# Kernel optimization log

Measured on AMD Instinct MI355X. Metric: run time of the kernel, lower is better.

Reference implementation:

```python
import jax, jax.numpy as jnp
import numpy as np

M = 16       # learned queries
K = 64       # top-k sparse tokens
HEADS = 4    # attention heads
LN_EPS = 1e-5


def _l2norm(x, eps=1e-12):
    n = jnp.linalg.norm(x, axis=-1, keepdims=True)
    return x / jnp.maximum(n, eps)


def _layernorm(x, w, b):
    mu = x.mean(-1, keepdims=True)
    var = x.var(-1, keepdims=True)
    return (x - mu) * jax.lax.rsqrt(var + LN_EPS) * w + b


def setup_inputs() -> dict:
    key = jax.random.key(0)
    ks = jax.random.split(key, 12)
    B, N, C, T, TD, D = 4, 16384, 1024, 20, 512, 64
    s = lambda k, sh: jax.random.normal(k, sh, jnp.float32) * 0.02
    return {
        "image_features": jax.random.normal(ks[0], (B, N, C), jnp.float32),
        "text_features": jax.random.normal(ks[1], (B, T, TD), jnp.float32),
        "Wd": s(ks[2], (C, D)), "bd": jnp.zeros((D,), jnp.float32),
        "Wu": s(ks[3], (D, C)), "bu": jnp.zeros((C,), jnp.float32),
        "m_queries": jax.random.normal(ks[4], (1, M, D), jnp.float32),
        "Wq": s(ks[5], (D, D)), "bq": jnp.zeros((D,), jnp.float32),
        "Wk": s(ks[6], (D, D)), "bk": jnp.zeros((D,), jnp.float32),
        "Wv": s(ks[7], (D, D)), "bv": jnp.zeros((D,), jnp.float32),
        "Wo": s(ks[8], (D, D)), "bo": jnp.zeros((D,), jnp.float32),
        "ln_w": jnp.ones((D,), jnp.float32), "ln_b": jnp.zeros((D,), jnp.float32),
        "gamma": jnp.float32(0.1),
    }


def reference(image_features, text_features, Wd, bd, Wu, bu, m_queries,
              Wq, bq, Wk, bk, Wv, bv, Wo, bo, ln_w, ln_b, gamma):
    B, N, C = image_features.shape
    D = Wd.shape[1]
    identity = image_features

    # down-project + exact GELU (dropout is identity at eval)
    a = jax.nn.gelu(image_features @ Wd + bd, approximate=False)  # [B,N,D]

    # tokens_of_interest=None, text_consistency_loss=False:
    # slice text to projected dim, take token 0 as key
    sel = text_features[:, 0, :D]                                  # [B,D]
    scores = jnp.einsum("bnd,bd->bn", _l2norm(a), _l2norm(sel))    # [B,N]

    # top-k mask -> nonzero gives row-sorted indices per batch
    _, idx = jax.lax.top_k(scores, K)                              # [B,K]
    idx = jnp.sort(idx, axis=1)

    sparse = jnp.take_along_axis(a, idx[:, :, None], axis=1)       # [B,K,D]
    queries = jnp.broadcast_to(m_queries, (B, M, D))
    comb = jnp.concatenate([queries, sparse], axis=1)              # [B,M+K,D]

    x = _layernorm(comb, ln_w, ln_b)
    H, Dh = HEADS, D // HEADS
    S = M + K
    q = (x @ Wq + bq).reshape(B, S, H, Dh)
    k = (x @ Wk + bk).reshape(B, S, H, Dh)
    v = (x @ Wv + bv).reshape(B, S, H, Dh)
    att = jnp.einsum("bshd,bthd->bhst", q, k) / jnp.sqrt(jnp.float32(Dh))
    att = jax.nn.softmax(att, axis=-1)
    o = jnp.einsum("bhst,bthd->bshd", att, v).reshape(B, S, D)
    attn_out = o @ Wo + bo

    enh = comb + attn_out
    enh_sparse = enh[:, M:, :]                                     # [B,K,D]

    # scatter enhanced sparse tokens back into full sequence
    brow = jnp.arange(B)[:, None]
    delta_proj = jnp.zeros_like(a).at[brow, idx].set(enh_sparse)   # [B,N,D]
    delta_x = delta_proj @ Wu + bu                                 # [B,N,C]

    return identity + delta_x * gamma
```

## Files before the change

### kernel.cpp

```cpp
#include <hip/hip_runtime.h>
#include <hip/hip_bf16.h>
#include <math.h>

typedef __bf16 bf16x8 __attribute__((ext_vector_type(8)));
typedef unsigned short u16x8 __attribute__((ext_vector_type(8)));
typedef float f32x4 __attribute__((ext_vector_type(4)));

#define CDIM 1024
#define DDIM 64
#define NB   16384
#define NROWS 65536

__device__ __forceinline__ unsigned short f2bf(float x){
  unsigned int u = __float_as_uint(x);
  unsigned int lsb = (u >> 16) & 1u;
  u += 0x7fffu + lsb;
  return (unsigned short)(u >> 16);
}

__global__ __launch_bounds__(256) void dsa_prep(
    const float* __restrict__ Wd, const float* __restrict__ tf,
    const float* __restrict__ bu, const float* __restrict__ gam,
    unsigned short* __restrict__ Wf, float* __restrict__ seln,
    float* __restrict__ gbu){
  int bb = blockIdx.x, tid = threadIdx.x;
  if (bb < 32){
    int g = bb*256 + tid;
    int lane = g & 63, tj = g >> 6;
    int n  = ((tj & 3) << 4) + (lane & 15);
    int k0 = ((tj >> 2) << 5) + ((lane >> 4) << 3);
    u16x8 uv;
    #pragma unroll
    for (int e=0;e<8;e++) uv[e] = f2bf(Wd[(k0+e)*DDIM + n]);
    *(u16x8*)(Wf + (size_t)g*8) = uv;
  } else {
    int w = tid >> 6, lane = tid & 63;
    float x = tf[w*(20*512) + lane];
    float sq = x*x;
    #pragma unroll
    for (int m=1; m<64; m<<=1) sq += __shfl_xor(sq, m);
    seln[w*64 + lane] = x / fmaxf(sqrtf(sq), 1e-12f);
    float g = gam[0];
    f32x4 b4 = *(const f32x4*)(bu + tid*4);
    *(f32x4*)(gbu + tid*4) = g*b4;
  }
}

__global__ __launch_bounds__(256) void dsa_main(
    const float* __restrict__ X, const unsigned short* __restrict__ Wf,
    const float* __restrict__ bd, const float* __restrict__ gbu,
    const float* __restrict__ seln,
    float* __restrict__ out, float* __restrict__ a_out, float* __restrict__ scores)
{
  __shared__ __align__(16) float gbS[1024];
  const int tid  = threadIdx.x;
  const int lane = tid & 63, w = tid >> 6;
  const int lr = lane & 15, lq = lane >> 4;
  const int row0 = blockIdx.x*64 + w*16;
  const int batch = blockIdx.x >> 8;

  { f32x4 t = *(const f32x4*)(gbu + tid*4); *(f32x4*)(gbS + tid*4) = t; }
  __syncthreads();

  const float* xp = X   + (size_t)(row0 + lr)*CDIM + lq*8;
  float*       op = out + (size_t)(row0 + lr)*CDIM + lq*8;
  const bf16x8* wf8 = (const bf16x8*)Wf;

  f32x4  xa[3], xb[3];
  bf16x8 B[3][4];
  f32x4  acc[4] = {};

#define LDX(T) { xa[(T)%3] = *(const f32x4*)(xp + (T)*32); \
                 xb[(T)%3] = *(const f32x4*)(xp + (T)*32 + 4); }
#define LDBF(T) { B[(T)%3][0] = wf8[((T)*4+0)*64 + lane]; \
                  B[(T)%3][1] = wf8[((T)*4+1)*64 + lane]; \
                  B[(T)%3][2] = wf8[((T)*4+2)*64 + lane]; \
                  B[(T)%3][3] = wf8[((T)*4+3)*64 + lane]; }

  LDX(0) LDBF(0)
  LDX(1) LDBF(1)
  #pragma unroll
  for (int t = 0; t < 32; ++t){
    if (t + 2 < 32){ LDX(t+2) LDBF(t+2) }
    f32x4 g0 = *(const f32x4*)(gbS + t*32 + lq*8);
    f32x4 g1 = *(const f32x4*)(gbS + t*32 + lq*8 + 4);
    f32x4 va = xa[t%3], vb = xb[t%3];
    *(f32x4*)(op + t*32)     = va + g0;
    *(f32x4*)(op + t*32 + 4) = vb + g1;
    bf16x8 av;
    av[0]=(__bf16)va[0]; av[1]=(__bf16)va[1]; av[2]=(__bf16)va[2]; av[3]=(__bf16)va[3];
    av[4]=(__bf16)vb[0]; av[5]=(__bf16)vb[1]; av[6]=(__bf16)vb[2]; av[7]=(__bf16)vb[3];
    acc[0] = __builtin_amdgcn_mfma_f32_16x16x32_bf16(av, B[t%3][0], acc[0], 0,0,0);
    acc[1] = __builtin_amdgcn_mfma_f32_16x16x32_bf16(av, B[t%3][1], acc[1], 0,0,0);
    acc[2] = __builtin_amdgcn_mfma_f32_16x16x32_bf16(av, B[t%3][2], acc[2], 0,0,0);
    acc[3] = __builtin_amdgcn_mfma_f32_16x16x32_bf16(av, B[t%3][3], acc[3], 0,0,0);
  }
#undef LDX
#undef LDBF

  const float* selb = seln + batch*64;
  float ss[4] = {0,0,0,0}, dt[4] = {0,0,0,0};
  float gv[4][4];
  #pragma unroll
  for (int j=0;j<4;j++){
    int col = 16*j + lr;
    float bdc = bd[col];
    float sc  = selb[col];
    #pragma unroll
    for (int r=0;r<4;r++){
      float y = acc[j][r] + bdc;
      float g = 0.5f * y * (1.0f + erff(y * 0.70710678118654752f));
      gv[j][r] = g;
      ss[r] += g*g;
      dt[r] += g*sc;
    }
  }
  #pragma unroll
  for (int r=0;r<4;r++){
    int row = row0 + 4*lq + r;
    #pragma unroll
    for (int j=0;j<4;j++)
      a_out[(size_t)row*DDIM + 16*j + lr] = gv[j][r];
  }
  #pragma unroll
  for (int m=1;m<16;m<<=1){
    #pragma unroll
    for (int r=0;r<4;r++){
      ss[r] += __shfl_xor(ss[r], m);
      dt[r] += __shfl_xor(dt[r], m);
    }
  }
  if (lr == 0){
    #pragma unroll
    for (int r=0;r<4;r++)
      scores[row0 + 4*lq + r] = dt[r] / fmaxf(sqrtf(ss[r]), 1e-12f);
  }
}

__global__ __launch_bounds__(1024) void dsa_topk(const float* __restrict__ scores,
                                                 int* __restrict__ idxo){
  const int b = blockIdx.x, tid = threadIdx.x;
  const float* s = scores + b*NB;
  const int base = tid*16;
  unsigned key[16];
  #pragma unroll
  for (int i=0;i<16;i+=4){
    f32x4 f = *(const f32x4*)(s + base + i);
    #pragma unroll
    for (int c=0;c<4;c++){
      unsigned u = __float_as_uint(f[c]);
      key[i+c] = (u & 0x80000000u) ? ~u : (u | 0x80000000u);
    }
  }

  __shared__ unsigned bins[256];
  __shared__ unsigned sh_pref, sh_R;
  __shared__ int selIdx[64];
  __shared__ int eqIdx[256];
  __shared__ unsigned selCnt, eqCnt;

  unsigned prefix = 0, R = 64;
  for (int pass=0; pass<4; ++pass){
    const int shift = 24 - pass*8;
    if (tid < 256) bins[tid] = 0;
    __syncthreads();
    #pragma unroll
    for (int i=0;i<16;i++){
      unsigned k = key[i];
      bool ok;
      if (pass == 0) ok = true;
      else           ok = ((k >> (shift+8)) == prefix);
      if (ok) atomicAdd(&bins[(k >> shift) & 255u], 1u);
    }
    __syncthreads();
    if (tid < 64){
      unsigned c0 = bins[tid*4+0], c1 = bins[tid*4+1];
      unsigned c2 = bins[tid*4+2], c3 = bins[tid*4+3];
      unsigned gs = c0+c1+c2+c3;
      unsigned suf = gs;
      #pragma unroll
      for (int m=1;m<64;m<<=1){
        unsigned o = __shfl_down(suf, m);
        if (tid + m < 64) suf += o;
      }
      unsigned above = suf - gs;
      if (above < R && R <= suf){
        unsigned a3 = above;
        unsigned a2 = a3 + c3;
        unsigned a1 = a2 + c2;
        unsigned a0 = a1 + c1;
        unsigned bb, ab;
        if      (R <= a3 + c3){ bb = 3; ab = a3; }
        else if (R <= a2 + c2){ bb = 2; ab = a2; }
        else if (R <= a1 + c1){ bb = 1; ab = a1; }
        else                  { bb = 0; ab = a0; }
        sh_pref = (prefix << 8) | (tid*4 + bb);
        sh_R = R - ab;
      }
    }
    __syncthreads();
    prefix = sh_pref; R = sh_R;
    __syncthreads();
  }
  if (tid == 0){ selCnt = 0; eqCnt = 0; }
  __syncthreads();
  #pragma unroll
  for (int i=0;i<16;i++){
    unsigned k = key[i];
    if (k > prefix){
      selIdx[atomicAdd(&selCnt, 1u)] = base + i;
    } else if (k == prefix){
      unsigned p = atomicAdd(&eqCnt, 1u);
      if (p < 256) eqIdx[p] = base + i;
    }
  }
  __syncthreads();
  if (tid == 0){
    unsigned n = eqCnt < 256u ? eqCnt : 256u;
    unsigned have = selCnt;
    for (unsigned r2 = 0; r2 < R; ++r2){
      int best = 0x7fffffff, bi = -1;
      for (unsigned e=0; e<n; e++)
        if (eqIdx[e] < best){ best = eqIdx[e]; bi = (int)e; }
      selIdx[have + r2] = best;
      eqIdx[bi] = 0x7fffffff;
    }
  }
  __syncthreads();
  if (tid < 64){
    int x = selIdx[tid];
    #pragma unroll
    for (int size=2; size<=64; size<<=1){
      #pragma unroll
      for (int stride=size>>1; stride>0; stride>>=1){
        int ox = __shfl_xor(x, stride);
        bool up = ((tid & size) == 0);
        bool takeMin = (((tid & stride) == 0) == up);
        int mn = x < ox ? x : ox, mx = x < ox ? ox : x;
        x = takeMin ? mn : mx;
      }
    }
    idxo[b*64 + tid] = x;
  }
}

__global__ __launch_bounds__(512) void dsa_tail(
    const float* __restrict__ a, const float* __restrict__ mq, const int* __restrict__ idx,
    const float* __restrict__ lnw, const float* __restrict__ lnb,
    const float* __restrict__ Wq, const float* __restrict__ bq,
    const float* __restrict__ Wk, const float* __restrict__ bk,
    const float* __restrict__ Wv, const float* __restrict__ bv,
    const float* __restrict__ Wo, const float* __restrict__ bo,
    float* __restrict__ enh)
{
  __shared__ float xln[80][64];
  __shared__ float qS[80][64];
  __shared__ float vS[80][68];
  __shared__ float kT[64][81];
  __shared__ float oS[80][64];
  __shared__ float WoS[64][64];
  __shared__ float rowbuf[8][84];
  __shared__ int   sidx[64];

  const int b = blockIdx.x, tid = threadIdx.x;
  const int w = tid >> 6, lane = tid & 63;

  if (tid < 64) sidx[tid] = idx[b*64 + tid];
  for (int e = tid; e < 4096; e += 512) WoS[e>>6][e&63] = Wo[e];
  __syncthreads();

  {
    float lw = lnw[lane], lb = lnb[lane];
    float vals[10];
    #pragma unroll
    for (int i=0;i<10;i++){
      int s = w + 8*i;
      vals[i] = (s < 16) ? mq[s*64 + lane]
                         : a[((size_t)b*NB + sidx[s-16])*64 + lane];
    }
    #pragma unroll
    for (int i=0;i<10;i++){
      int s = w + 8*i;
      float val = vals[i];
      float sm = val, sq = val*val;
      #pragma unroll
      for (int m=1;m<64;m<<=1){ sm += __shfl_xor(sm,m); sq += __shfl_xor(sq,m); }
      float mu  = sm * (1.0f/64.0f);
      float var = sq * (1.0f/64.0f) - mu*mu;
      xln[s][lane] = (val - mu) * rsqrtf(var + 1e-5f) * lw + lb;
    }
  }
  __syncthreads();

  #pragma unroll 1
  for (int m = 0; m < 3; ++m){
    const float* Wm = (m==0) ? Wq : (m==1) ? Wk : Wv;
    const float* bm = (m==0) ? bq : (m==1) ? bk : bv;
    float wreg[64];
    #pragma unroll
    for (int c=0;c<64;c++) wreg[c] = Wm[c*64 + lane];
    float bias = bm[lane];
    #pragma unroll 1
    for (int s = w; s < 80; s += 8){
      float accv = bias;
      #pragma unroll
      for (int c4=0;c4<16;c4++){
        f32x4 x4 = *(const f32x4*)&xln[s][c4*4];
        accv += x4[0]*wreg[c4*4+0] + x4[1]*wreg[c4*4+1]
              + x4[2]*wreg[c4*4+2] + x4[3]*wreg[c4*4+3];
      }
      if (m==0)      qS[s][lane]  = accv;
      else if (m==1) kT[lane][s]  = accv;
      else           vS[s][lane]  = accv;
    }
  }
  __syncthreads();

  {
    const int h = w >> 1, h16 = h*16;
    const int i0 = 16 + (w & 1)*32;
    const int jj = lane >> 4, dd = lane & 15;
    #pragma unroll 2
    for (int ii = 0; ii < 32; ++ii){
      int i = i0 + ii;
      float v0 = 0.f, v1 = 0.f;
      #pragma unroll
      for (int d=0; d<16; ++d){
        float qd = qS[i][h16+d];
        v0 = fmaf(qd, kT[h16+d][lane],    v0);
        v1 = fmaf(qd, kT[h16+d][64 + dd], v1);
      }
      v0 *= 0.25f; v1 *= 0.25f;
      float mx = fmaxf(v0, v1);
      #pragma unroll
      for (int m2=1;m2<64;m2<<=1) mx = fmaxf(mx, __shfl_xor(mx,m2));
      float e0 = expf(v0 - mx);
      float e1 = expf(v1 - mx);
      float sm = e0 + ((lane < 16) ? e1 : 0.f);
      #pragma unroll
      for (int m2=1;m2<64;m2<<=1) sm += __shfl_xor(sm,m2);
      float inv = 1.0f / sm;
      rowbuf[w][lane] = e0 * inv;
      if (lane < 16) rowbuf[w][64+dd] = e1 * inv;
      float part = 0.f;
      #pragma unroll
      for (int tt=0; tt<20; ++tt){
        int j = jj*20 + tt;
        part = fmaf(rowbuf[w][j], vS[j][h16+dd], part);
      }
      part += __shfl_xor(part, 16);
      part += __shfl_xor(part, 32);
      if (lane < 16) oS[i][h16+dd] = part;
    }
  }
  __syncthreads();

  for (int e = tid; e < 4096; e += 512){
    int s16 = e >> 6, cc = e & 63;
    float accv = bo[cc];
    #pragma unroll
    for (int d4=0; d4<16; ++d4){
      f32x4 o4 = *(const f32x4*)&oS[16+s16][d4*4];
      accv += o4[0]*WoS[d4*4+0][cc] + o4[1]*WoS[d4*4+1][cc]
            + o4[2]*WoS[d4*4+2][cc] + o4[3]*WoS[d4*4+3][cc];
    }
    float cmb = a[((size_t)b*NB + sidx[s16])*64 + cc];
    enh[(b*64 + s16)*64 + cc] = cmb + accv;
  }
}

__global__ __launch_bounds__(256) void dsa_scatter(
    const float* __restrict__ enh, const float* __restrict__ Wu,
    const float* __restrict__ gam, const int* __restrict__ idx,
    float* __restrict__ out)
{
  int blk = blockIdx.x;
  int b = blk >> 6, j = blk & 63;
  int tid = threadIdx.x;
  __shared__ float er[64];
  if (tid < 64) er[tid] = enh[(b*64+j)*64 + tid];
  __syncthreads();
  int n = idx[b*64 + j];
  float gamma = gam[0];
  int c0 = tid*4;
  float ax=0.f, ay=0.f, az=0.f, aw=0.f;
  #pragma unroll 8
  for (int d=0; d<64; ++d){
    float ev = er[d];
    f32x4 wr = *(const f32x4*)(Wu + d*CDIM + c0);
    ax += ev*wr[0]; ay += ev*wr[1]; az += ev*wr[2]; aw += ev*wr[3];
  }
  float* op = out + ((size_t)b*NB + n)*CDIM + c0;
  f32x4 cu = *(f32x4*)op;
  cu[0] += gamma*ax; cu[1] += gamma*ay; cu[2] += gamma*az; cu[3] += gamma*aw;
  *(f32x4*)op = cu;
}

extern "C" void kernel_launch(void* const* d_in, const int* in_sizes, int n_in,
                              void* d_out, int out_size, void* d_ws, size_t ws_size,
                              hipStream_t stream) {
  const float* X    = (const float*)d_in[0];
  const float* tf   = (const float*)d_in[1];
  const float* Wd   = (const float*)d_in[2];
  const float* bd   = (const float*)d_in[3];
  const float* Wu   = (const float*)d_in[4];
  const float* bu   = (const float*)d_in[5];
  const float* mq   = (const float*)d_in[6];
  const float* Wq   = (const float*)d_in[7];
  const float* bq   = (const float*)d_in[8];
  const float* Wk   = (const float*)d_in[9];
  const float* bk   = (const float*)d_in[10];
  const float* Wv   = (const float*)d_in[11];
  const float* bv   = (const float*)d_in[12];
  const float* Wo   = (const float*)d_in[13];
  const float* bo   = (const float*)d_in[14];
  const float* lnw  = (const float*)d_in[15];
  const float* lnb  = (const float*)d_in[16];
  const float* gam  = (const float*)d_in[17];
  float* out = (float*)d_out;

  float* ws_a               = (float*)d_ws;
  unsigned short* ws_wf     = (unsigned short*)(ws_a + (size_t)NROWS*DDIM);
  float* ws_scores          = (float*)(ws_wf + 64*CDIM);
  float* ws_seln            = ws_scores + NROWS;
  float* ws_gbu             = ws_seln + 256;
  int*   ws_idx             = (int*)(ws_gbu + 1024);
  float* ws_enh             = (float*)(ws_idx + 256);

  dsa_prep   <<<33,   256, 0, stream>>>(Wd, tf, bu, gam, ws_wf, ws_seln, ws_gbu);
  dsa_main   <<<1024, 256, 0, stream>>>(X, ws_wf, bd, ws_gbu, ws_seln,
                                        out, ws_a, ws_scores);
  dsa_topk   <<<4,   1024, 0, stream>>>(ws_scores, ws_idx);
  dsa_tail   <<<4,    512, 0, stream>>>(ws_a, mq, ws_idx, lnw, lnb,
                                        Wq, bq, Wk, bk, Wv, bv, Wo, bo, ws_enh);
  dsa_scatter<<<256,  256, 0, stream>>>(ws_enh, Wu, gam, ws_idx, out);
}
```

Before: 240.8 us.

## Stage X tiles through LDS with coalesced row-contiguous loads for MFMA

The main streaming kernel now loads X with each group of 8 lanes covering a contiguous 128-float span of a row, instead of the MFMA fragment layout that had each lane read 8 floats at strided offsets. Each tile is converted to bf16 and written into a double-buffered per-wave LDS tile, from which the MFMA operands are read. The bias add and output store use the same coalesced layout, and gamma*bu is read directly from global memory rather than from shared memory. This aims for better-coalesced HBM reads and writes and sets launch bounds for 4 blocks per CU, at the cost of extra LDS traffic and explicit lgkmcnt waits. It also adds an LDS wait in the attention kernel.

```diff
diff --git a/kernel.cpp b/kernel.cpp
--- a/kernel.cpp
+++ b/kernel.cpp
@@ -3,6 +3,7 @@
 #include <math.h>
 
 typedef __bf16 bf16x8 __attribute__((ext_vector_type(8)));
+typedef __bf16 bf16x4 __attribute__((ext_vector_type(4)));
 typedef unsigned short u16x8 __attribute__((ext_vector_type(8)));
 typedef float f32x4 __attribute__((ext_vector_type(4)));
 
@@ -46,57 +47,95 @@
   }
 }
 
-__global__ __launch_bounds__(256) void dsa_main(
+__global__ __launch_bounds__(256, 4) void dsa_main(
     const float* __restrict__ X, const unsigned short* __restrict__ Wf,
     const float* __restrict__ bd, const float* __restrict__ gbu,
     const float* __restrict__ seln,
     float* __restrict__ out, float* __restrict__ a_out, float* __restrict__ scores)
 {
-  __shared__ __align__(16) float gbS[1024];
+  __shared__ __align__(16) unsigned short Abuf[4][2][16*136];
   const int tid  = threadIdx.x;
   const int lane = tid & 63, w = tid >> 6;
   const int lr = lane & 15, lq = lane >> 4;
   const int row0 = blockIdx.x*64 + w*16;
   const int batch = blockIdx.x >> 8;
-
-  { f32x4 t = *(const f32x4*)(gbu + tid*4); *(f32x4*)(gbS + tid*4) = t; }
-  __syncthreads();
-
-  const float* xp = X   + (size_t)(row0 + lr)*CDIM + lq*8;
-  float*       op = out + (size_t)(row0 + lr)*CDIM + lq*8;
+  const int r8 = lane >> 3, ck = lane & 7;
+
+  const float* xbase = X   + (size_t)row0*CDIM;
+  float*       obase = out + (size_t)row0*CDIM;
   const bf16x8* wf8 = (const bf16x8*)Wf;
-
-  f32x4  xa[3], xb[3];
-  bf16x8 B[3][4];
+  unsigned short* lds = &Abuf[w][0][0];
+
+  f32x4  xr[2][4];
+  f32x4  g[4];
+  bf16x8 Bb[2][4];
   f32x4  acc[4] = {};
 
-#define LDX(T) { xa[(T)%3] = *(const f32x4*)(xp + (T)*32); \
-                 xb[(T)%3] = *(const f32x4*)(xp + (T)*32 + 4); }
-#define LDBF(T) { B[(T)%3][0] = wf8[((T)*4+0)*64 + lane]; \
-                  B[(T)%3][1] = wf8[((T)*4+1)*64 + lane]; \
-                  B[(T)%3][2] = wf8[((T)*4+2)*64 + lane]; \
-                  B[(T)%3][3] = wf8[((T)*4+3)*64 + lane]; }
-
-  LDX(0) LDBF(0)
-  LDX(1) LDBF(1)
-  #pragma unroll
-  for (int t = 0; t < 32; ++t){
-    if (t + 2 < 32){ LDX(t+2) LDBF(t+2) }
-    f32x4 g0 = *(const f32x4*)(gbS + t*32 + lq*8);
-    f32x4 g1 = *(const f32x4*)(gbS + t*32 + lq*8 + 4);
-    f32x4 va = xa[t%3], vb = xb[t%3];
-    *(f32x4*)(op + t*32)     = va + g0;
-    *(f32x4*)(op + t*32 + 4) = vb + g1;
-    bf16x8 av;
-    av[0]=(__bf16)va[0]; av[1]=(__bf16)va[1]; av[2]=(__bf16)va[2]; av[3]=(__bf16)va[3];
-    av[4]=(__bf16)vb[0]; av[5]=(__bf16)vb[1]; av[6]=(__bf16)vb[2]; av[7]=(__bf16)vb[3];
-    acc[0] = __builtin_amdgcn_mfma_f32_16x16x32_bf16(av, B[t%3][0], acc[0], 0,0,0);
-    acc[1] = __builtin_amdgcn_mfma_f32_16x16x32_bf16(av, B[t%3][1], acc[1], 0,0,0);
-    acc[2] = __builtin_amdgcn_mfma_f32_16x16x32_bf16(av, B[t%3][2], acc[2], 0,0,0);
-    acc[3] = __builtin_amdgcn_mfma_f32_16x16x32_bf16(av, B[t%3][3], acc[3], 0,0,0);
-  }
-#undef LDX
-#undef LDBF
+#define LBUF(P) (lds + (((P)&1)*(16*136)))
+
+#define ISSUE_X(P) { \
+  const float* xq = xbase + (P)*128; \
+  xr[0][0]=*(const f32x4*)(xq + (size_t)(r8  )*CDIM + (ck+ 0)*4); \
+  xr[0][1]=*(const f32x4*)(xq + (size_t)(r8  )*CDIM + (ck+ 8)*4); \
+  xr[0][2]=*(const f32x4*)(xq + (size_t)(r8  )*CDIM + (ck+16)*4); \
+  xr[0][3]=*(const f32x4*)(xq + (size_t)(r8  )*CDIM + (ck+24)*4); \
+  xr[1][0]=*(const f32x4*)(xq + (size_t)(r8+8)*CDIM + (ck+ 0)*4); \
+  xr[1][1]=*(const f32x4*)(xq + (size_t)(r8+8)*CDIM + (ck+ 8)*4); \
+  xr[1][2]=*(const f32x4*)(xq + (size_t)(r8+8)*CDIM + (ck+16)*4); \
+  xr[1][3]=*(const f32x4*)(xq + (size_t)(r8+8)*CDIM + (ck+24)*4); \
+  g[0]=*(const f32x4*)(gbu + (P)*128 + (ck+ 0)*4); \
+  g[1]=*(const f32x4*)(gbu + (P)*128 + (ck+ 8)*4); \
+  g[2]=*(const f32x4*)(gbu + (P)*128 + (ck+16)*4); \
+  g[3]=*(const f32x4*)(gbu + (P)*128 + (ck+24)*4); }
+
+#define ST1(P, LP, H, J, RR) { \
+  f32x4 o = xr[H][J] + g[J]; \
+  *(f32x4*)(obase + (size_t)(RR)*CDIM + (P)*128 + (ck+8*(J))*4) = o; \
+  bf16x4 bv; \
+  bv[0]=(__bf16)xr[H][J][0]; bv[1]=(__bf16)xr[H][J][1]; \
+  bv[2]=(__bf16)xr[H][J][2]; bv[3]=(__bf16)xr[H][J][3]; \
+  *(bf16x4*)((LP) + (RR)*136 + (ck+8*(J))*4) = bv; }
+
+#define STORE_STAGE(P, LP) { \
+  ST1(P, LP, 0, 0, r8)   ST1(P, LP, 0, 1, r8)   ST1(P, LP, 0, 2, r8)   ST1(P, LP, 0, 3, r8) \
+  ST1(P, LP, 1, 0, r8+8) ST1(P, LP, 1, 1, r8+8) ST1(P, LP, 1, 2, r8+8) ST1(P, LP, 1, 3, r8+8) }
+
+#define LDB(T, I) { \
+  Bb[I][0] = wf8[((T)*4+0)*64 + lane]; \
+  Bb[I][1] = wf8[((T)*4+1)*64 + lane]; \
+  Bb[I][2] = wf8[((T)*4+2)*64 + lane]; \
+  Bb[I][3] = wf8[((T)*4+3)*64 + lane]; }
+
+#define KSTEP(T, K0, P) { \
+  if ((T)+1 < 32) LDB((T)+1, ((T)+1)&1) \
+  bf16x8 av = *(const bf16x8*)(LBUF(P) + lr*136 + (K0)*32 + lq*8); \
+  acc[0] = __builtin_amdgcn_mfma_f32_16x16x32_bf16(av, Bb[(T)&1][0], acc[0], 0,0,0); \
+  acc[1] = __builtin_amdgcn_mfma_f32_16x16x32_bf16(av, Bb[(T)&1][1], acc[1], 0,0,0); \
+  acc[2] = __builtin_amdgcn_mfma_f32_16x16x32_bf16(av, Bb[(T)&1][2], acc[2], 0,0,0); \
+  acc[3] = __builtin_amdgcn_mfma_f32_16x16x32_bf16(av, Bb[(T)&1][3], acc[3], 0,0,0); }
+
+#define PH(P) { \
+  asm volatile("s_waitcnt lgkmcnt(0)" ::: "memory"); \
+  __builtin_amdgcn_sched_barrier(0); \
+  KSTEP(4*(P)+0, 0, P) KSTEP(4*(P)+1, 1, P) \
+  KSTEP(4*(P)+2, 2, P) KSTEP(4*(P)+3, 3, P) \
+  if ((P) < 7) STORE_STAGE((P)+1, LBUF((P)+1)) \
+  if ((P) < 6) ISSUE_X((P)+2) }
+
+  ISSUE_X(0)
+  STORE_STAGE(0, LBUF(0))
+  ISSUE_X(1)
+  LDB(0, 0)
+
+  PH(0) PH(1) PH(2) PH(3) PH(4) PH(5) PH(6) PH(7)
+
+#undef LBUF
+#undef ISSUE_X
+#undef ST1
+#undef STORE_STAGE
+#undef LDB
+#undef KSTEP
+#undef PH
 
   const float* selb = seln + batch*64;
   float ss[4] = {0,0,0,0}, dt[4] = {0,0,0,0};
@@ -109,10 +148,10 @@
     #pragma unroll
     for (int r=0;r<4;r++){
       float y = acc[j][r] + bdc;
-      float g = 0.5f * y * (1.0f + erff(y * 0.70710678118654752f));
-      gv[j][r] = g;
-      ss[r] += g*g;
-      dt[r] += g*sc;
+      float gg = 0.5f * y * (1.0f + erff(y * 0.70710678118654752f));
+      gv[j][r] = gg;
+      ss[r] += gg*gg;
+      dt[r] += gg*sc;
     }
   }
   #pragma unroll
@@ -342,6 +381,7 @@
       float inv = 1.0f / sm;
       rowbuf[w][lane] = e0 * inv;
       if (lane < 16) rowbuf[w][64+dd] = e1 * inv;
+      asm volatile("s_waitcnt lgkmcnt(0)" ::: "memory");
       float part = 0.f;
       #pragma unroll
       for (int tt=0; tt<20; ++tt){
```

After: 237.4 us. Within noise of the previous version (-1.4%).

## Stage X rows through swizzled LDS with coalesced row-contiguous loads

Applied to the files above, without the earlier changes.

The main streaming loop now has each wave load 16 full rows of X in 256-column panels. Each lane reads a contiguous float4, so a wave covers one row segment, instead of strided per-lane row reads. The wave writes out+gamma*bu directly, converts the panel to bf16 into an XOR-swizzled LDS buffer, and reads MFMA A-fragments back from LDS while the next panel's global loads are in flight. This aims to improve global-memory coalescing and overlap the stream with the MFMAs. In exchange it uses 32KB of LDS and 16 float4 staging registers, which may lower occupancy. It also adds explicit waitcnt and sched_barrier fences, plus one in the attention code.

```diff
diff --git a/kernel.cpp b/kernel.cpp
--- a/kernel.cpp
+++ b/kernel.cpp
@@ -3,6 +3,7 @@
 #include <math.h>
 
 typedef __bf16 bf16x8 __attribute__((ext_vector_type(8)));
+typedef __bf16 bf16x4 __attribute__((ext_vector_type(4)));
 typedef unsigned short u16x8 __attribute__((ext_vector_type(8)));
 typedef float f32x4 __attribute__((ext_vector_type(4)));
 
@@ -52,51 +53,74 @@
     const float* __restrict__ seln,
     float* __restrict__ out, float* __restrict__ a_out, float* __restrict__ scores)
 {
-  __shared__ __align__(16) float gbS[1024];
+  __shared__ __align__(16) unsigned short Abuf[4][4096];
   const int tid  = threadIdx.x;
   const int lane = tid & 63, w = tid >> 6;
   const int lr = lane & 15, lq = lane >> 4;
   const int row0 = blockIdx.x*64 + w*16;
   const int batch = blockIdx.x >> 8;
-
-  { f32x4 t = *(const f32x4*)(gbu + tid*4); *(f32x4*)(gbS + tid*4) = t; }
-  __syncthreads();
-
-  const float* xp = X   + (size_t)(row0 + lr)*CDIM + lq*8;
-  float*       op = out + (size_t)(row0 + lr)*CDIM + lq*8;
+  const int xmask = (lr & 7) << 3;
+
+  const float* xb = X   + (size_t)row0*CDIM;
+  float*       ob = out + (size_t)row0*CDIM;
   const bf16x8* wf8 = (const bf16x8*)Wf;
-
-  f32x4  xa[3], xb[3];
-  bf16x8 B[3][4];
+  unsigned short* lds = &Abuf[w][0];
+
+  f32x4  xr[16];
+  f32x4  g;
+  bf16x8 Bb[2][4];
   f32x4  acc[4] = {};
 
-#define LDX(T) { xa[(T)%3] = *(const f32x4*)(xp + (T)*32); \
-                 xb[(T)%3] = *(const f32x4*)(xp + (T)*32 + 4); }
-#define LDBF(T) { B[(T)%3][0] = wf8[((T)*4+0)*64 + lane]; \
-                  B[(T)%3][1] = wf8[((T)*4+1)*64 + lane]; \
-                  B[(T)%3][2] = wf8[((T)*4+2)*64 + lane]; \
-                  B[(T)%3][3] = wf8[((T)*4+3)*64 + lane]; }
-
-  LDX(0) LDBF(0)
-  LDX(1) LDBF(1)
-  #pragma unroll
-  for (int t = 0; t < 32; ++t){
-    if (t + 2 < 32){ LDX(t+2) LDBF(t+2) }
-    f32x4 g0 = *(const f32x4*)(gbS + t*32 + lq*8);
-    f32x4 g1 = *(const f32x4*)(gbS + t*32 + lq*8 + 4);
-    f32x4 va = xa[t%3], vb = xb[t%3];
-    *(f32x4*)(op + t*32)     = va + g0;
-    *(f32x4*)(op + t*32 + 4) = vb + g1;
-    bf16x8 av;
-    av[0]=(__bf16)va[0]; av[1]=(__bf16)va[1]; av[2]=(__bf16)va[2]; av[3]=(__bf16)va[3];
-    av[4]=(__bf16)vb[0]; av[5]=(__bf16)vb[1]; av[6]=(__bf16)vb[2]; av[7]=(__bf16)vb[3];
-    acc[0] = __builtin_amdgcn_mfma_f32_16x16x32_bf16(av, B[t%3][0], acc[0], 0,0,0);
-    acc[1] = __builtin_amdgcn_mfma_f32_16x16x32_bf16(av, B[t%3][1], acc[1], 0,0,0);
-    acc[2] = __builtin_amdgcn_mfma_f32_16x16x32_bf16(av, B[t%3][2], acc[2], 0,0,0);
-    acc[3] = __builtin_amdgcn_mfma_f32_16x16x32_bf16(av, B[t%3][3], acc[3], 0,0,0);
-  }
-#undef LDX
-#undef LDBF
+  auto issue_x = [&](int P){
+    #pragma unroll
+    for (int i=0;i<16;i++)
+      xr[i] = *(const f32x4*)(xb + (size_t)i*CDIM + P*256 + lane*4);
+    g = *(const f32x4*)(gbu + P*256 + lane*4);
+  };
+  auto out_cvt_write = [&](int P){
+    #pragma unroll
+    for (int i=0;i<16;i++){
+      f32x4 o = xr[i] + g;
+      *(f32x4*)(ob + (size_t)i*CDIM + P*256 + lane*4) = o;
+      bf16x4 bv;
+      bv[0]=(__bf16)xr[i][0]; bv[1]=(__bf16)xr[i][1];
+      bv[2]=(__bf16)xr[i][2]; bv[3]=(__bf16)xr[i][3];
+      *(bf16x4*)(lds + i*256 + ((lane*4) ^ ((i&7)<<3))) = bv;
+    }
+  };
+
+  issue_x(0);
+  out_cvt_write(0);
+  Bb[0][0] = wf8[0*64 + lane];
+  Bb[0][1] = wf8[1*64 + lane];
+  Bb[0][2] = wf8[2*64 + lane];
+  Bb[0][3] = wf8[3*64 + lane];
+
+  #pragma unroll
+  for (int P = 0; P < 4; ++P){
+    asm volatile("s_waitcnt lgkmcnt(0)" ::: "memory");
+    __builtin_amdgcn_sched_barrier(0);
+    if (P < 3) issue_x(P+1);
+    #pragma unroll
+    for (int t = 0; t < 8; ++t){
+      int kk = P*8 + t;
+      if (t < 7 || P < 3){
+        Bb[(t+1)&1][0] = wf8[((kk+1)*4+0)*64 + lane];
+        Bb[(t+1)&1][1] = wf8[((kk+1)*4+1)*64 + lane];
+        Bb[(t+1)&1][2] = wf8[((kk+1)*4+2)*64 + lane];
+        Bb[(t+1)&1][3] = wf8[((kk+1)*4+3)*64 + lane];
+      }
+      int cidx = (t*32 + lq*8) ^ xmask;
+      bf16x8 av = *(const bf16x8*)(lds + lr*256 + cidx);
+      acc[0] = __builtin_amdgcn_mfma_f32_16x16x32_bf16(av, Bb[t&1][0], acc[0], 0,0,0);
+      acc[1] = __builtin_amdgcn_mfma_f32_16x16x32_bf16(av, Bb[t&1][1], acc[1], 0,0,0);
+      acc[2] = __builtin_amdgcn_mfma_f32_16x16x32_bf16(av, Bb[t&1][2], acc[2], 0,0,0);
+      acc[3] = __builtin_amdgcn_mfma_f32_16x16x32_bf16(av, Bb[t&1][3], acc[3], 0,0,0);
+    }
+    asm volatile("s_waitcnt lgkmcnt(0)" ::: "memory");
+    __builtin_amdgcn_sched_barrier(0);
+    if (P < 3) out_cvt_write(P+1);
+  }
 
   const float* selb = seln + batch*64;
   float ss[4] = {0,0,0,0}, dt[4] = {0,0,0,0};
@@ -109,10 +133,10 @@
     #pragma unroll
     for (int r=0;r<4;r++){
       float y = acc[j][r] + bdc;
-      float g = 0.5f * y * (1.0f + erff(y * 0.70710678118654752f));
-      gv[j][r] = g;
-      ss[r] += g*g;
-      dt[r] += g*sc;
+      float gg = 0.5f * y * (1.0f + erff(y * 0.70710678118654752f));
+      gv[j][r] = gg;
+      ss[r] += gg*gg;
+      dt[r] += gg*sc;
     }
   }
   #pragma unroll
@@ -342,6 +366,7 @@
       float inv = 1.0f / sm;
       rowbuf[w][lane] = e0 * inv;
       if (lane < 16) rowbuf[w][64+dd] = e1 * inv;
+      asm volatile("s_waitcnt lgkmcnt(0)" ::: "memory");
       float part = 0.f;
       #pragma unroll
       for (int tt=0; tt<20; ++tt){
```

Result: faster. 215.0 us (-10.7%).

## Split K dimension across wave pairs in main GEMM kernel and double grid

Applied to the files above, without the earlier changes.

Each block now handles 32 rows instead of 64. Pairs of waves split the 1024-wide reduction in half, and the partial MFMA accumulators are combined through shared memory, so twice as many blocks launch. The explicit triple-buffered register prefetch is removed and launch bounds request 8 blocks per CU, aiming for more memory parallelism through occupancy rather than software pipelining. A waitcnt is also added in the tail softmax before rowbuf is read. The cost is extra shared memory, a block-wide barrier, and half the waves sitting idle during the epilogue.

```diff
diff --git a/kernel.cpp b/kernel.cpp
--- a/kernel.cpp
+++ b/kernel.cpp
@@ -46,57 +46,68 @@
   }
 }
 
-__global__ __launch_bounds__(256) void dsa_main(
+__global__ __launch_bounds__(256, 8) void dsa_main(
     const float* __restrict__ X, const unsigned short* __restrict__ Wf,
     const float* __restrict__ bd, const float* __restrict__ gbu,
     const float* __restrict__ seln,
     float* __restrict__ out, float* __restrict__ a_out, float* __restrict__ scores)
 {
   __shared__ __align__(16) float gbS[1024];
+  __shared__ float accS[2][1024];
   const int tid  = threadIdx.x;
   const int lane = tid & 63, w = tid >> 6;
+  const int rg = w >> 1, kh = w & 1;
   const int lr = lane & 15, lq = lane >> 4;
-  const int row0 = blockIdx.x*64 + w*16;
-  const int batch = blockIdx.x >> 8;
-
-  { f32x4 t = *(const f32x4*)(gbu + tid*4); *(f32x4*)(gbS + tid*4) = t; }
-  __syncthreads();
-
-  const float* xp = X   + (size_t)(row0 + lr)*CDIM + lq*8;
-  float*       op = out + (size_t)(row0 + lr)*CDIM + lq*8;
+  const int row0 = blockIdx.x*32 + rg*16;
+  const int batch = blockIdx.x >> 9;
+
+  { f32x4 t4 = *(const f32x4*)(gbu + tid*4); *(f32x4*)(gbS + tid*4) = t4; }
+  __syncthreads();
+
+  const size_t rowoff = (size_t)(row0 + lr)*CDIM + kh*512 + lq*8;
+  const float* xp = X   + rowoff;
+  float*       op = out + rowoff;
   const bf16x8* wf8 = (const bf16x8*)Wf;
-
-  f32x4  xa[3], xb[3];
-  bf16x8 B[3][4];
-  f32x4  acc[4] = {};
-
-#define LDX(T) { xa[(T)%3] = *(const f32x4*)(xp + (T)*32); \
-                 xb[(T)%3] = *(const f32x4*)(xp + (T)*32 + 4); }
-#define LDBF(T) { B[(T)%3][0] = wf8[((T)*4+0)*64 + lane]; \
-                  B[(T)%3][1] = wf8[((T)*4+1)*64 + lane]; \
-                  B[(T)%3][2] = wf8[((T)*4+2)*64 + lane]; \
-                  B[(T)%3][3] = wf8[((T)*4+3)*64 + lane]; }
-
-  LDX(0) LDBF(0)
-  LDX(1) LDBF(1)
-  #pragma unroll
-  for (int t = 0; t < 32; ++t){
-    if (t + 2 < 32){ LDX(t+2) LDBF(t+2) }
-    f32x4 g0 = *(const f32x4*)(gbS + t*32 + lq*8);
-    f32x4 g1 = *(const f32x4*)(gbS + t*32 + lq*8 + 4);
-    f32x4 va = xa[t%3], vb = xb[t%3];
-    *(f32x4*)(op + t*32)     = va + g0;
-    *(f32x4*)(op + t*32 + 4) = vb + g1;
+  const int gb0 = kh*512 + lq*8;
+
+  f32x4 acc[4] = {};
+
+  #pragma unroll
+  for (int t = 0; t < 16; ++t){
+    f32x4 xa = *(const f32x4*)(xp + t*32);
+    f32x4 xb = *(const f32x4*)(xp + t*32 + 4);
+    const int tg = kh*16 + t;
+    bf16x8 b0 = wf8[(tg*4+0)*64 + lane];
+    bf16x8 b1 = wf8[(tg*4+1)*64 + lane];
+    bf16x8 b2 = wf8[(tg*4+2)*64 + lane];
+    bf16x8 b3 = wf8[(tg*4+3)*64 + lane];
+    f32x4 g0 = *(const f32x4*)(gbS + gb0 + t*32);
+    f32x4 g1 = *(const f32x4*)(gbS + gb0 + t*32 + 4);
+    *(f32x4*)(op + t*32)     = xa + g0;
+    *(f32x4*)(op + t*32 + 4) = xb + g1;
     bf16x8 av;
-    av[0]=(__bf16)va[0]; av[1]=(__bf16)va[1]; av[2]=(__bf16)va[2]; av[3]=(__bf16)va[3];
-    av[4]=(__bf16)vb[0]; av[5]=(__bf16)vb[1]; av[6]=(__bf16)vb[2]; av[7]=(__bf16)vb[3];
-    acc[0] = __builtin_amdgcn_mfma_f32_16x16x32_bf16(av, B[t%3][0], acc[0], 0,0,0);
-    acc[1] = __builtin_amdgcn_mfma_f32_16x16x32_bf16(av, B[t%3][1], acc[1], 0,0,0);
-    acc[2] = __builtin_amdgcn_mfma_f32_16x16x32_bf16(av, B[t%3][2], acc[2], 0,0,0);
-    acc[3] = __builtin_amdgcn_mfma_f32_16x16x32_bf16(av, B[t%3][3], acc[3], 0,0,0);
-  }
-#undef LDX
-#undef LDBF
+    av[0]=(__bf16)xa[0]; av[1]=(__bf16)xa[1]; av[2]=(__bf16)xa[2]; av[3]=(__bf16)xa[3];
+    av[4]=(__bf16)xb[0]; av[5]=(__bf16)xb[1]; av[6]=(__bf16)xb[2]; av[7]=(__bf16)xb[3];
+    acc[0] = __builtin_amdgcn_mfma_f32_16x16x32_bf16(av, b0, acc[0], 0,0,0);
+    acc[1] = __builtin_amdgcn_mfma_f32_16x16x32_bf16(av, b1, acc[1], 0,0,0);
+    acc[2] = __builtin_amdgcn_mfma_f32_16x16x32_bf16(av, b2, acc[2], 0,0,0);
+    acc[3] = __builtin_amdgcn_mfma_f32_16x16x32_bf16(av, b3, acc[3], 0,0,0);
+  }
+
+  if (kh == 1){
+    #pragma unroll
+    for (int j=0;j<4;j++)
+      #pragma unroll
+      for (int r=0;r<4;r++)
+        accS[rg][lane + 64*(j*4+r)] = acc[j][r];
+  }
+  __syncthreads();
+  if (kh == 1) return;
+  #pragma unroll
+  for (int j=0;j<4;j++)
+    #pragma unroll
+    for (int r=0;r<4;r++)
+      acc[j][r] += accS[rg][lane + 64*(j*4+r)];
 
   const float* selb = seln + batch*64;
   float ss[4] = {0,0,0,0}, dt[4] = {0,0,0,0};
@@ -109,10 +120,10 @@
     #pragma unroll
     for (int r=0;r<4;r++){
       float y = acc[j][r] + bdc;
-      float g = 0.5f * y * (1.0f + erff(y * 0.70710678118654752f));
-      gv[j][r] = g;
-      ss[r] += g*g;
-      dt[r] += g*sc;
+      float gg = 0.5f * y * (1.0f + erff(y * 0.70710678118654752f));
+      gv[j][r] = gg;
+      ss[r] += gg*gg;
+      dt[r] += gg*sc;
     }
   }
   #pragma unroll
@@ -342,6 +353,7 @@
       float inv = 1.0f / sm;
       rowbuf[w][lane] = e0 * inv;
       if (lane < 16) rowbuf[w][64+dd] = e1 * inv;
+      asm volatile("s_waitcnt lgkmcnt(0)" ::: "memory");
       float part = 0.f;
       #pragma unroll
       for (int tt=0; tt<20; ++tt){
@@ -428,7 +440,7 @@
   float* ws_enh             = (float*)(ws_idx + 256);
 
   dsa_prep   <<<33,   256, 0, stream>>>(Wd, tf, bu, gam, ws_wf, ws_seln, ws_gbu);
-  dsa_main   <<<1024, 256, 0, stream>>>(X, ws_wf, bd, ws_gbu, ws_seln,
+  dsa_main   <<<2048, 256, 0, stream>>>(X, ws_wf, bd, ws_gbu, ws_seln,
                                         out, ws_a, ws_scores);
   dsa_topk   <<<4,   1024, 0, stream>>>(ws_scores, ws_idx);
   dsa_tail   <<<4,    512, 0, stream>>>(ws_a, mq, ws_idx, lnw, lnb,
```

Result: faster. 235.2 us (-2.3%).
